# Kernel tuning notes

Hardware: AMD Instinct MI355X
Metric: run time of the kernel (lower is better)

## Reference

```python
import jax, jax.numpy as jnp
import numpy as np

E = 1024  # embed_dim
H = 16    # num_heads
D = E // H  # head_dim


def setup_inputs() -> dict:
    key = jax.random.key(0)
    ks = jax.random.split(key, 9)
    s = 0.02
    return {
        "hidden_state": jax.random.normal(ks[0], (4, 1024, E), jnp.float32),
        "Wq": jax.random.normal(ks[1], (H, D, E), jnp.float32) * s,
        "bq": jax.random.normal(ks[2], (H, D), jnp.float32) * s,
        "Wk": jax.random.normal(ks[3], (H, D, E), jnp.float32) * s,
        "bk": jax.random.normal(ks[4], (H, D), jnp.float32) * s,
        "Wv": jax.random.normal(ks[5], (H, D, E), jnp.float32) * s,
        "bv": jax.random.normal(ks[6], (H, D), jnp.float32) * s,
        "Wo": jax.random.normal(ks[7], (E, E), jnp.float32) * s,
        "bo": jax.random.normal(ks[8], (E,), jnp.float32) * s,
    }


def _mha(x, Wq, bq, Wk, bk, Wv, bv, Wo, bo):
    # Per-head linear projections (torch Linear: y = x W^T + b), batched over heads.
    q = jnp.einsum("bse,hde->bhsd", x, Wq) + bq[None, :, None, :]
    k = jnp.einsum("bse,hde->bhsd", x, Wk) + bk[None, :, None, :]
    v = jnp.einsum("bse,hde->bhsd", x, Wv) + bv[None, :, None, :]
    scores = jnp.einsum("bhsd,bhtd->bhst", q, k) / jnp.sqrt(jnp.asarray(D, x.dtype))
    w = jax.nn.softmax(scores, axis=-1)  # F.softmax default -> last dim
    o = jnp.einsum("bhst,bhtd->bhsd", w, v)
    # concat heads along last dim: [B,S,H*D] in head order (matches torch.cat)
    B, _, S, _ = o.shape
    o = jnp.transpose(o, (0, 2, 1, 3)).reshape(B, S, H * D)
    return o @ Wo.T + bo


def reference(hidden_state, Wq, bq, Wk, bk, Wv, bv, Wo, bo):
    return _mha(hidden_state, Wq, bq, Wk, bk, Wv, bv, Wo, bo)
```

## Files before the change

kernel.cpp:

```cpp
#include <hip/hip_runtime.h>
#include <hip/hip_bf16.h>
#include <stdint.h>

#define E_DIM 1024
#define H_NUM 16
#define D_DIM 64
#define B_NUM 4
#define S_LEN 1024

typedef __attribute__((ext_vector_type(8))) short bf16x8;
typedef __attribute__((ext_vector_type(4))) short bf16x4;
typedef __attribute__((ext_vector_type(4))) float f32x4;

#define SOFTMAX_C2 0.18033688011112042f

__device__ inline ushort f2b(float x) {
    __hip_bfloat16 h = __float2bfloat16(x);
    return *(ushort*)&h;
}
__device__ inline float b2f(ushort u) {
    __hip_bfloat16 h = *(__hip_bfloat16*)&u;
    return __bfloat162float(h);
}
__device__ inline uint pk2(float a, float b) {
    __hip_bfloat162 h = __float22bfloat162_rn(make_float2(a, b));
    return *(uint*)&h;
}

__device__ inline void gld16(const ushort* g, ushort* l) {
    __builtin_amdgcn_global_load_lds((const __attribute__((address_space(1))) void*)g,
                                     (__attribute__((address_space(3))) void*)l, 16, 0, 0);
}

__global__ __launch_bounds__(256)
void convert_all(const float* __restrict__ X,  const float* __restrict__ Wq,
                 const float* __restrict__ Wk, const float* __restrict__ Wv,
                 const float* __restrict__ Wo,
                 ushort* __restrict__ Xb, ushort* __restrict__ Wcat,
                 ushort* __restrict__ Wob)
{
    const int bid = blockIdx.x;
    const float* src; ushort* dst; size_t off;
    if (bid < 4096)      { src = X;  dst = Xb;   off = (size_t)bid * 1024; }
    else if (bid < 5120) { src = Wq; dst = Wcat;              off = (size_t)(bid - 4096) * 1024; }
    else if (bid < 6144) { src = Wk; dst = Wcat + (1u << 20); off = (size_t)(bid - 5120) * 1024; }
    else if (bid < 7168) { src = Wv; dst = Wcat + (2u << 20); off = (size_t)(bid - 6144) * 1024; }
    else                 { src = Wo; dst = Wob;               off = (size_t)(bid - 7168) * 1024; }
    const size_t i = off + (size_t)threadIdx.x * 4;
    float4 v = *(const float4*)&src[i];
    ushort4 o;
    o.x = f2b(v.x); o.y = f2b(v.y); o.z = f2b(v.z); o.w = f2b(v.w);
    *(ushort4*)&dst[i] = o;
}

__global__ __launch_bounds__(256, 3)
void gemm_qkv(const ushort* __restrict__ A, const ushort* __restrict__ Bw,
              const float* __restrict__ b0, const float* __restrict__ b1,
              const float* __restrict__ b2,
              ushort* __restrict__ Qb, ushort* __restrict__ Kb,
              ushort* __restrict__ Vt_g, int K)
{
    __shared__ __align__(16) ushort SM[24576];
    ushort* As = SM;
    ushort* Bs = SM + 16384;

    const int tid  = threadIdx.x;
    const int wave = tid >> 6;
    const int lane = tid & 63;
    const int quad = lane >> 4;
    const int l16  = lane & 15;
    const int wm   = wave & 1;
    const int wn   = wave >> 1;
    const int m0   = blockIdx.x * 128;
    const int n0   = blockIdx.y * 64;

    f32x4 acc[4][2] = {};

    auto stageA = [&](int buf, int k0) {
#pragma unroll
        for (int i = 0; i < 4; ++i) {
            const int e   = i * 256 + tid;
            const int row = e >> 3;
            const int gc8 = ((e & 7) ^ (row & 7)) * 8;
            gld16(&A[(size_t)(m0 + row) * K + k0 + gc8], &As[buf * 8192 + e * 8]);
        }
    };
    auto stageB = [&](int buf, int k0) {
#pragma unroll
        for (int i = 0; i < 2; ++i) {
            const int e   = i * 256 + tid;
            const int row = e >> 3;
            const int gc8 = ((e & 7) ^ (row & 7)) * 8;
            gld16(&Bw[(size_t)(n0 + row) * K + k0 + gc8], &Bs[buf * 4096 + e * 8]);
        }
    };

    stageA(0, 0); stageB(0, 0);
    __syncthreads();

    const int nk = K >> 6;
    const int xa = (l16 & 7) * 8;
    for (int ki = 0; ki < nk; ++ki) {
        const int cur = ki & 1;
        if (ki + 1 < nk) { stageA(cur ^ 1, (ki + 1) << 6); stageB(cur ^ 1, (ki + 1) << 6); }

#pragma unroll
        for (int ks = 0; ks < 2; ++ks) {
            const int lc = (ks * 32 + quad * 8) ^ xa;
            bf16x8 af[4], bf[2];
#pragma unroll
            for (int mi = 0; mi < 4; ++mi)
                af[mi] = *(const bf16x8*)&As[cur * 8192 + (wm * 64 + mi * 16 + l16) * 64 + lc];
#pragma unroll
            for (int ni = 0; ni < 2; ++ni)
                bf[ni] = *(const bf16x8*)&Bs[cur * 4096 + (wn * 32 + ni * 16 + l16) * 64 + lc];
#pragma unroll
            for (int mi = 0; mi < 4; ++mi)
#pragma unroll
                for (int ni = 0; ni < 2; ++ni)
                    acc[mi][ni] = __builtin_amdgcn_mfma_f32_16x16x32_bf16(af[mi], bf[ni], acc[mi][ni], 0, 0, 0);
        }
        __syncthreads();
    }

    const int seg   = n0 >> 10;
    const int cbase = n0 & 1023;
    const float* bp = (seg == 0) ? b0 : (seg == 1) ? b1 : b2;
    const float scl = (seg == 0) ? SOFTMAX_C2 : 1.0f;

    if (seg < 2) {
        ushort* T = SM;
#pragma unroll
        for (int ni = 0; ni < 2; ++ni) {
            const int nloc = wn * 32 + ni * 16 + l16;
            const float bv = bp[cbase + nloc];
#pragma unroll
            for (int mi = 0; mi < 4; ++mi)
#pragma unroll
                for (int r = 0; r < 4; ++r)
                    T[(wm * 64 + mi * 16 + quad * 4 + r) * 72 + nloc] =
                        f2b((acc[mi][ni][r] + bv) * scl);
        }
        __syncthreads();
        ushort* dst = (seg == 0) ? Qb : Kb;
        const int row = tid >> 1, half = tid & 1;
        const ushort* s = &T[row * 72 + half * 32];
        ushort* d = &dst[(size_t)(m0 + row) * 1024 + cbase + half * 32];
#pragma unroll
        for (int j = 0; j < 4; ++j)
            *(uint4*)(d + j * 8) = *(const uint4*)(s + j * 8);
    } else {
        ushort* Tt = SM;
        const int hh = cbase >> 6;
        const int b  = m0 >> 10, sbase = m0 & 1023;
#pragma unroll
        for (int ni = 0; ni < 2; ++ni) {
            const int nloc = wn * 32 + ni * 16 + l16;
            const float bv = bp[cbase + nloc];
#pragma unroll
            for (int mi = 0; mi < 4; ++mi) {
                const int mloc = wm * 64 + mi * 16 + quad * 4;
                ushort4 pk;
                pk.x = f2b(acc[mi][ni][0] + bv);
                pk.y = f2b(acc[mi][ni][1] + bv);
                pk.z = f2b(acc[mi][ni][2] + bv);
                pk.w = f2b(acc[mi][ni][3] + bv);
                *(ushort4*)&Tt[nloc * 136 + mloc] = pk;
            }
        }
        __syncthreads();
        const int nrow = tid >> 2, qtr = tid & 3;
        const ushort* s = &Tt[nrow * 136 + qtr * 32];
        ushort* d = &Vt_g[(((size_t)(b * 16 + hh)) * 64 + nrow) * 1024 + sbase + qtr * 32];
#pragma unroll
        for (int j = 0; j < 4; ++j)
            *(uint4*)(d + j * 8) = *(const uint4*)(s + j * 8);
    }
}

__global__ __launch_bounds__(256, 8)
void attention7(const ushort* __restrict__ Qg, const ushort* __restrict__ Kg,
                const ushort* __restrict__ Vg,
                ushort* __restrict__ Opart, float* __restrict__ Lpart)
{
    __shared__ __align__(16) ushort SM[9216];

    const int tid  = threadIdx.x;
    const int w    = tid >> 6;
    const int lane = tid & 63;
    const int quad = lane >> 4;
    const int l16  = lane & 15;

    const int gid = blockIdx.x;
    const int qt  = (gid >> 3) & 15;
    const int grp = (gid & 7) | ((gid >> 7) << 3);
    const int bh  = grp & 63;
    const int th  = grp >> 6;
    const int b   = bh >> 4;
    const int h   = bh & 15;
    const size_t tbase = ((size_t)b * S_LEN) * E_DIM + (size_t)h * D_DIM;
    const size_t vbase = (size_t)bh * D_DIM * S_LEN;
    const int t0 = th * 512;

    const ushort* qrow = Qg + tbase + (size_t)(qt * 64 + w * 16 + l16) * E_DIM + quad * 8;
    bf16x8 qf[2];
    qf[0] = *(const bf16x8*)qrow;
    qf[1] = *(const bf16x8*)(qrow + 32);

    const int krow = tid >> 3, kslot = tid & 7;
    const int vr   = tid >> 2, vc = (tid & 3) * 8;

    auto stageK = [&](int buf, int tg) {
        gld16(&Kg[tbase + (size_t)(tg + krow) * E_DIM + ((kslot ^ (krow & 7)) * 8)],
              &SM[buf * 2048 + tid * 8]);
    };

    stageK(0, t0);
    {
        uint4 v0 = *(const uint4*)&Vg[vbase + (size_t)vr * S_LEN + t0 + vc];
        *(uint4*)&SM[4096 + vr * 40 + vc] = v0;
    }
    __syncthreads();

    float lq = 0.0f;
    f32x4 oacc[4] = {};
    const int xk = (l16 & 7);

    for (int kt = 0; kt < 16; ++kt) {
        const int cur = kt & 1;

        uint4 vpre;
        if (kt < 15) {
            const int tg = t0 + (kt + 1) * 32;
            stageK(cur ^ 1, tg);
            vpre = *(const uint4*)&Vg[vbase + (size_t)vr * S_LEN + tg + vc];
        }

        f32x4 sacc[2] = {};
#pragma unroll
        for (int mt = 0; mt < 2; ++mt)
#pragma unroll
            for (int ks = 0; ks < 2; ++ks) {
                bf16x8 kf = *(const bf16x8*)&SM[cur * 2048 + (mt * 16 + l16) * 64 +
                                                (((ks * 4 + quad) ^ xk) * 8)];
                sacc[mt] = __builtin_amdgcn_mfma_f32_16x16x32_bf16(kf, qf[ks], sacc[mt], 0, 0, 0);
            }

        bf16x4 pf[2];
        float rs = 0.0f;
#pragma unroll
        for (int mt = 0; mt < 2; ++mt) {
            float p0 = exp2f(sacc[mt][0]);
            float p1 = exp2f(sacc[mt][1]);
            float p2 = exp2f(sacc[mt][2]);
            float p3 = exp2f(sacc[mt][3]);
            rs += (p0 + p1) + (p2 + p3);
            union { uint uu[2]; bf16x4 v; } pk;
            pk.uu[0] = pk2(p0, p1);
            pk.uu[1] = pk2(p2, p3);
            pf[mt] = pk.v;
        }
        lq += rs;

#pragma unroll
        for (int nb = 0; nb < 4; ++nb)
#pragma unroll
            for (int kb = 0; kb < 2; ++kb) {
                bf16x4 vf = *(const bf16x4*)&SM[4096 + cur * 2560 +
                                                (nb * 16 + l16) * 40 + kb * 16 + quad * 4];
                oacc[nb] = __builtin_amdgcn_mfma_f32_16x16x16bf16_1k(pf[kb], vf, oacc[nb], 0, 0, 0);
            }

        if (kt < 15)
            *(uint4*)&SM[4096 + (cur ^ 1) * 2560 + vr * 40 + vc] = vpre;
        __syncthreads();
    }

    lq += __shfl_xor(lq, 16);
    lq += __shfl_xor(lq, 32);
    const size_t obase = ((size_t)(th * 64 + bh)) * S_LEN;
    if (lane < 16)
        Lpart[obase + qt * 64 + w * 16 + l16] = lq;

    ushort* T = SM;
#pragma unroll
    for (int nb = 0; nb < 4; ++nb)
#pragma unroll
        for (int r = 0; r < 4; ++r)
            T[(w * 16 + quad * 4 + r) * 72 + nb * 16 + l16] = f2b(oacc[nb][r]);
    __syncthreads();
    {
        const int row = tid >> 2, c16 = (tid & 3) * 16;
        const ushort* s = &T[row * 72 + c16];
        ushort* d = &Opart[(obase + qt * 64 + row) * 64 + c16];
        *(uint4*)(d)     = *(const uint4*)(s);
        *(uint4*)(d + 8) = *(const uint4*)(s + 8);
    }
}

__global__ __launch_bounds__(256, 4)
void gemm_out(const ushort* __restrict__ Opart, const float* __restrict__ Lpart,
              const ushort* __restrict__ Bw, const float* __restrict__ bias,
              float* __restrict__ Cout)
{
    __shared__ __align__(16) ushort SM[17408];
    ushort* As = SM;
    ushort* Bs = SM + 9216;

    const int tid  = threadIdx.x;
    const int w    = tid >> 6;
    const int lane = tid & 63;
    const int quad = lane >> 4;
    const int l16  = lane & 15;
    const int m0   = blockIdx.x * 64;
    const int n0   = blockIdx.y * 64;

    const int arow = tid >> 2;
    const int acol = (tid & 3) * 16;
    const int m    = m0 + arow;
    const int ab   = m >> 10;
    const int as   = m & 1023;

    f32x4 acc[4] = {};

    auto loadA = [&](int ki, uint4* o0, uint4* o1, float* linv) {
        const int bh = ab * 16 + ki;
        const size_t p0 = ((size_t)bh * 1024 + as) * 64 + acol;
        const size_t p1 = ((size_t)(64 + bh) * 1024 + as) * 64 + acol;
#pragma unroll
        for (int j = 0; j < 2; ++j) {
            o0[j] = *(const uint4*)&Opart[p0 + j * 8];
            o1[j] = *(const uint4*)&Opart[p1 + j * 8];
        }
        const float l0 = Lpart[(size_t)bh * 1024 + as];
        const float l1 = Lpart[(size_t)(64 + bh) * 1024 + as];
        *linv = 1.0f / (l0 + l1);
    };
    auto writeA = [&](int buf, const uint4* o0, const uint4* o1, float linv) {
        ushort* dst = &As[buf * 4608 + arow * 72 + acol];
#pragma unroll
        for (int j = 0; j < 2; ++j) {
            const ushort* a = (const ushort*)&o0[j];
            const ushort* c = (const ushort*)&o1[j];
            union { uint uu[4]; uint4 v; } pk;
            pk.uu[0] = pk2((b2f(a[0]) + b2f(c[0])) * linv, (b2f(a[1]) + b2f(c[1])) * linv);
            pk.uu[1] = pk2((b2f(a[2]) + b2f(c[2])) * linv, (b2f(a[3]) + b2f(c[3])) * linv);
            pk.uu[2] = pk2((b2f(a[4]) + b2f(c[4])) * linv, (b2f(a[5]) + b2f(c[5])) * linv);
            pk.uu[3] = pk2((b2f(a[6]) + b2f(c[6])) * linv, (b2f(a[7]) + b2f(c[7])) * linv);
            *(uint4*)(dst + j * 8) = pk.v;
        }
    };
    auto stageB = [&](int buf, int k0) {
#pragma unroll
        for (int i = 0; i < 2; ++i) {
            const int e   = i * 256 + tid;
            const int row = e >> 3;
            const int gc8 = ((e & 7) ^ (row & 7)) * 8;
            gld16(&Bw[(size_t)(n0 + row) * 1024 + k0 + gc8], &Bs[buf * 4096 + e * 8]);
        }
    };

    {
        uint4 o0[2], o1[2]; float linv;
        loadA(0, o0, o1, &linv);
        writeA(0, o0, o1, linv);
        stageB(0, 0);
    }
    __syncthreads();

    const int xa = (l16 & 7) * 8;
    for (int ki = 0; ki < 16; ++ki) {
        const int cur = ki & 1;

        uint4 o0[2], o1[2]; float linv;
        if (ki + 1 < 16) {
            loadA(ki + 1, o0, o1, &linv);
            stageB(cur ^ 1, (ki + 1) << 6);
        }

#pragma unroll
        for (int ks = 0; ks < 2; ++ks) {
            bf16x8 af = *(const bf16x8*)&As[cur * 4608 + (w * 16 + l16) * 72 + ks * 32 + quad * 8];
#pragma unroll
            for (int nb = 0; nb < 4; ++nb) {
                const int lcB = (ks * 32 + quad * 8) ^ xa;
                bf16x8 bf = *(const bf16x8*)&Bs[cur * 4096 + (nb * 16 + l16) * 64 + lcB];
                acc[nb] = __builtin_amdgcn_mfma_f32_16x16x32_bf16(af, bf, acc[nb], 0, 0, 0);
            }
        }

        if (ki + 1 < 16) writeA(cur ^ 1, o0, o1, linv);
        __syncthreads();
    }

    float* Tf = (float*)SM;
#pragma unroll
    for (int nb = 0; nb < 4; ++nb) {
        const float bv = bias[n0 + nb * 16 + l16];
#pragma unroll
        for (int r = 0; r < 4; ++r)
            Tf[(w * 16 + quad * 4 + r) * 68 + nb * 16 + l16] = acc[nb][r] + bv;
    }
    __syncthreads();
    {
        const int row = tid >> 2, c16 = (tid & 3) * 16;
        const float* s = &Tf[row * 68 + c16];
        float* d = &Cout[(size_t)(m0 + row) * 1024 + n0 + c16];
#pragma unroll
        for (int j = 0; j < 4; ++j)
            *(float4*)(d + j * 4) = *(const float4*)(s + j * 4);
    }
}

extern "C" void kernel_launch(void* const* d_in, const int* in_sizes, int n_in,
                              void* d_out, int out_size, void* d_ws, size_t ws_size,
                              hipStream_t stream)
{
    (void)in_sizes; (void)n_in; (void)out_size; (void)ws_size;

    const float* X  = (const float*)d_in[0];
    const float* Wq = (const float*)d_in[1];
    const float* bq = (const float*)d_in[2];
    const float* Wk = (const float*)d_in[3];
    const float* bk = (const float*)d_in[4];
    const float* Wv = (const float*)d_in[5];
    const float* bv = (const float*)d_in[6];
    const float* Wo = (const float*)d_in[7];
    const float* bo = (const float*)d_in[8];

    const size_t MEG = 1u << 20;
    ushort* ws    = (ushort*)d_ws;
    ushort* Xb    = ws;
    ushort* Wcat  = ws + 4 * MEG;
    ushort* Wob   = ws + 7 * MEG;
    ushort* Qb    = ws + 8 * MEG;
    ushort* Kb    = ws + 12 * MEG;
    ushort* Vtg   = ws + 16 * MEG;
    ushort* Opart = ws + 20 * MEG;
    float*  Lpart = (float*)(ws + 28 * MEG);

    dim3 blk(256);

    convert_all<<<8192, blk, 0, stream>>>(X, Wq, Wk, Wv, Wo, Xb, Wcat, Wob);

    gemm_qkv<<<dim3(32, 48), blk, 0, stream>>>(Xb, Wcat, bq, bk, bv,
                                               Qb, Kb, Vtg, E_DIM);

    attention7<<<2048, blk, 0, stream>>>(Qb, Kb, Vtg, Opart, Lpart);

    gemm_out<<<dim3(64, 16), blk, 0, stream>>>(Opart, Lpart, Wob, bo,
                                               (float*)d_out);
}
```

Baseline: 187.4 us.

## Process two query tiles per attention block to reuse staged K/V

Each attention block now handles 128 query rows (two 64-row tiles) instead of 64. Every K/V tile loaded into shared memory feeds twice as many MFMAs, and the grid shrinks from 2048 to 1024 blocks. The aim is to halve K/V global and LDS staging traffic and the barrier count per unit of work. In exchange register pressure roughly doubles for accumulators, launch bounds drop to 4 blocks per SM, and fewer blocks may reduce latency hiding.

Measured after the change: 191.4 us. 2.1% more time.

```diff
diff --git a/kernel.cpp b/kernel.cpp
--- a/kernel.cpp
+++ b/kernel.cpp
@@ -178,8 +178,8 @@
     }
 }
 
-__global__ __launch_bounds__(256, 8)
-void attention7(const ushort* __restrict__ Qg, const ushort* __restrict__ Kg,
+__global__ __launch_bounds__(256, 4)
+void attention8(const ushort* __restrict__ Qg, const ushort* __restrict__ Kg,
                 const ushort* __restrict__ Vg,
                 ushort* __restrict__ Opart, float* __restrict__ Lpart)
 {
@@ -192,8 +192,8 @@
     const int l16  = lane & 15;
 
     const int gid = blockIdx.x;
-    const int qt  = (gid >> 3) & 15;
-    const int grp = (gid & 7) | ((gid >> 7) << 3);
+    const int qt  = (gid >> 3) & 7;
+    const int grp = (gid & 7) | ((gid >> 6) << 3);
     const int bh  = grp & 63;
     const int th  = grp >> 6;
     const int b   = bh >> 4;
@@ -202,10 +202,14 @@
     const size_t vbase = (size_t)bh * D_DIM * S_LEN;
     const int t0 = th * 512;
 
-    const ushort* qrow = Qg + tbase + (size_t)(qt * 64 + w * 16 + l16) * E_DIM + quad * 8;
-    bf16x8 qf[2];
-    qf[0] = *(const bf16x8*)qrow;
-    qf[1] = *(const bf16x8*)(qrow + 32);
+    bf16x8 qf[2][2];
+#pragma unroll
+    for (int u = 0; u < 2; ++u) {
+        const ushort* qrow = Qg + tbase +
+            (size_t)(qt * 128 + u * 64 + w * 16 + l16) * E_DIM + quad * 8;
+        qf[u][0] = *(const bf16x8*)qrow;
+        qf[u][1] = *(const bf16x8*)(qrow + 32);
+    }
 
     const int krow = tid >> 3, kslot = tid & 7;
     const int vr   = tid >> 2, vc = (tid & 3) * 8;
@@ -222,8 +226,8 @@
     }
     __syncthreads();
 
-    float lq = 0.0f;
-    f32x4 oacc[4] = {};
+    float lq[2] = {0.0f, 0.0f};
+    f32x4 oacc[2][4] = {};
     const int xk = (l16 & 7);
 
     for (int kt = 0; kt < 16; ++kt) {
@@ -236,31 +240,35 @@
             vpre = *(const uint4*)&Vg[vbase + (size_t)vr * S_LEN + tg + vc];
         }
 
-        f32x4 sacc[2] = {};
+        f32x4 sacc[2][2] = {};
 #pragma unroll
         for (int mt = 0; mt < 2; ++mt)
 #pragma unroll
             for (int ks = 0; ks < 2; ++ks) {
                 bf16x8 kf = *(const bf16x8*)&SM[cur * 2048 + (mt * 16 + l16) * 64 +
                                                 (((ks * 4 + quad) ^ xk) * 8)];
-                sacc[mt] = __builtin_amdgcn_mfma_f32_16x16x32_bf16(kf, qf[ks], sacc[mt], 0, 0, 0);
+                sacc[0][mt] = __builtin_amdgcn_mfma_f32_16x16x32_bf16(kf, qf[0][ks], sacc[0][mt], 0, 0, 0);
+                sacc[1][mt] = __builtin_amdgcn_mfma_f32_16x16x32_bf16(kf, qf[1][ks], sacc[1][mt], 0, 0, 0);
             }
 
-        bf16x4 pf[2];
-        float rs = 0.0f;
-#pragma unroll
-        for (int mt = 0; mt < 2; ++mt) {
-            float p0 = exp2f(sacc[mt][0]);
-            float p1 = exp2f(sacc[mt][1]);
-            float p2 = exp2f(sacc[mt][2]);
-            float p3 = exp2f(sacc[mt][3]);
-            rs += (p0 + p1) + (p2 + p3);
-            union { uint uu[2]; bf16x4 v; } pk;
-            pk.uu[0] = pk2(p0, p1);
-            pk.uu[1] = pk2(p2, p3);
-            pf[mt] = pk.v;
-        }
-        lq += rs;
+        bf16x4 pf[2][2];
+#pragma unroll
+        for (int u = 0; u < 2; ++u) {
+            float rs = 0.0f;
+#pragma unroll
+            for (int mt = 0; mt < 2; ++mt) {
+                float p0 = exp2f(sacc[u][mt][0]);
+                float p1 = exp2f(sacc[u][mt][1]);
+                float p2 = exp2f(sacc[u][mt][2]);
+                float p3 = exp2f(sacc[u][mt][3]);
+                rs += (p0 + p1) + (p2 + p3);
+                union { uint uu[2]; bf16x4 v; } pk;
+                pk.uu[0] = pk2(p0, p1);
+                pk.uu[1] = pk2(p2, p3);
+                pf[u][mt] = pk.v;
+            }
+            lq[u] += rs;
+        }
 
 #pragma unroll
         for (int nb = 0; nb < 4; ++nb)
@@ -268,7 +276,8 @@
             for (int kb = 0; kb < 2; ++kb) {
                 bf16x4 vf = *(const bf16x4*)&SM[4096 + cur * 2560 +
                                                 (nb * 16 + l16) * 40 + kb * 16 + quad * 4];
-                oacc[nb] = __builtin_amdgcn_mfma_f32_16x16x16bf16_1k(pf[kb], vf, oacc[nb], 0, 0, 0);
+                oacc[0][nb] = __builtin_amdgcn_mfma_f32_16x16x16bf16_1k(pf[0][kb], vf, oacc[0][nb], 0, 0, 0);
+                oacc[1][nb] = __builtin_amdgcn_mfma_f32_16x16x16bf16_1k(pf[1][kb], vf, oacc[1][nb], 0, 0, 0);
             }
 
         if (kt < 15)
@@ -276,25 +285,31 @@
         __syncthreads();
     }
 
-    lq += __shfl_xor(lq, 16);
-    lq += __shfl_xor(lq, 32);
     const size_t obase = ((size_t)(th * 64 + bh)) * S_LEN;
-    if (lane < 16)
-        Lpart[obase + qt * 64 + w * 16 + l16] = lq;
-
-    ushort* T = SM;
-#pragma unroll
-    for (int nb = 0; nb < 4; ++nb)
-#pragma unroll
-        for (int r = 0; r < 4; ++r)
-            T[(w * 16 + quad * 4 + r) * 72 + nb * 16 + l16] = f2b(oacc[nb][r]);
-    __syncthreads();
-    {
-        const int row = tid >> 2, c16 = (tid & 3) * 16;
-        const ushort* s = &T[row * 72 + c16];
-        ushort* d = &Opart[(obase + qt * 64 + row) * 64 + c16];
-        *(uint4*)(d)     = *(const uint4*)(s);
-        *(uint4*)(d + 8) = *(const uint4*)(s + 8);
+
+#pragma unroll
+    for (int u = 0; u < 2; ++u) {
+        float l = lq[u];
+        l += __shfl_xor(l, 16);
+        l += __shfl_xor(l, 32);
+        if (lane < 16)
+            Lpart[obase + qt * 128 + u * 64 + w * 16 + l16] = l;
+
+        ushort* T = SM;
+#pragma unroll
+        for (int nb = 0; nb < 4; ++nb)
+#pragma unroll
+            for (int r = 0; r < 4; ++r)
+                T[(w * 16 + quad * 4 + r) * 72 + nb * 16 + l16] = f2b(oacc[u][nb][r]);
+        __syncthreads();
+        {
+            const int row = tid >> 2, c16 = (tid & 3) * 16;
+            const ushort* s = &T[row * 72 + c16];
+            ushort* d = &Opart[(obase + qt * 128 + u * 64 + row) * 64 + c16];
+            *(uint4*)(d)     = *(const uint4*)(s);
+            *(uint4*)(d + 8) = *(const uint4*)(s + 8);
+        }
+        __syncthreads();
     }
 }
 
@@ -446,7 +461,7 @@
     gemm_qkv<<<dim3(32, 48), blk, 0, stream>>>(Xb, Wcat, bq, bk, bv,
                                                Qb, Kb, Vtg, E_DIM);
 
-    attention7<<<2048, blk, 0, stream>>>(Qb, Kb, Vtg, Opart, Lpart);
+    attention8<<<1024, blk, 0, stream>>>(Qb, Kb, Vtg, Opart, Lpart);
 
     gemm_out<<<dim3(64, 16), blk, 0, stream>>>(Opart, Lpart, Wob, bo,
                                                (float*)d_out);
```
